# Kernel tuning notes

Measured on AMD Instinct MI355X. Metric: run time of the kernel, lower is better.

The kernel has to match this reference:

```python
import jax, jax.numpy as jnp
import numpy as np

NUM_HEADS = 4
KEY_DIM = 128


def rel_to_abs(rel):
    # rel: [B, heads, L, ww, 2*ww-1] -> [B, heads, L, ww, ww]
    B, heads, L, ww, dim = rel.shape
    flat = rel.reshape(B, heads, L, ww * (2 * ww - 1))[:, :, :, ww - 1:-1]
    return flat.reshape(B, heads, L, ww, 2 * (ww - 1))[..., :ww]


def relative_logits(pos_q, pos_emb_w, pos_emb_h):
    # pos_q: [B, hh, ww, heads, kd]
    # width logits
    q_w = jnp.transpose(pos_q, (0, 3, 1, 2, 4))           # [B, heads, hh, ww, kd]
    rel_w = jnp.einsum('bhxyd,dr->bhxyr', q_w, pos_emb_w)  # [B, heads, hh, ww, 2ww-1]
    rel_w = rel_to_abs(rel_w)                              # [B, heads, hh, ww, ww]
    # height logits
    q_h = jnp.transpose(pos_q, (0, 3, 2, 1, 4))           # [B, heads, ww, hh, kd]
    rel_h = jnp.einsum('bhyxd,dr->bhyxr', q_h, pos_emb_h)  # [B, heads, ww, hh, 2hh-1]
    rel_h = rel_to_abs(rel_h)                              # [B, heads, ww, hh, hh]
    rel_h = jnp.transpose(rel_h, (0, 1, 3, 2, 4))          # [B, heads, hh, ww, hh]
    # broadcast-add: [B, heads, hh, ww, hh, ww]
    return rel_w[:, :, :, :, None, :] + rel_h[:, :, :, :, :, None]


def setup_inputs() -> dict:
    key = jax.random.key(0)
    ks = jax.random.split(key, 7)
    B, H, W, C = 8, 32, 32, 512
    emb = NUM_HEADS * KEY_DIM
    stddev = KEY_DIM ** (-0.5)
    return {
        'x': jax.random.normal(ks[0], (B, H, W, C), jnp.float32),
        'Wq': jax.random.normal(ks[1], (C, emb), jnp.float32) * 0.02,
        'Wk': jax.random.normal(ks[2], (C, emb), jnp.float32) * 0.02,
        'Wv': jax.random.normal(ks[3], (C, emb), jnp.float32) * 0.02,
        'Wo': jax.random.normal(ks[4], (emb, emb), jnp.float32) * 0.02,
        'pos_emb_w': jax.random.normal(ks[5], (KEY_DIM, 2 * W - 1), jnp.float32) * stddev,
        'pos_emb_h': jax.random.normal(ks[6], (KEY_DIM, 2 * H - 1), jnp.float32) * stddev,
    }


def reference(x, Wq, Wk, Wv, Wo, pos_emb_w, pos_emb_h):
    B, hh, ww, C = x.shape
    heads, kd = NUM_HEADS, KEY_DIM
    L = hh * ww
    scale = 1.0 / jnp.sqrt(jnp.asarray(kd, x.dtype))

    q = (x @ Wq) * scale                                    # [B, hh, ww, heads*kd]
    attn_q = q.reshape(B, L, heads, kd).transpose(0, 2, 1, 3)   # [B, heads, L, kd]
    pos_q = q.reshape(B, hh, ww, heads, kd)
    k = (x @ Wk).reshape(B, L, heads, kd).transpose(0, 2, 3, 1)  # [B, heads, kd, L]
    v = (x @ Wv).reshape(B, L, heads, kd).transpose(0, 2, 1, 3)  # [B, heads, L, kd]

    scores = attn_q @ k                                      # [B, heads, L, L]
    pos = relative_logits(pos_q, pos_emb_w, pos_emb_h)        # [B, heads, hh, ww, hh, ww]
    scores = scores + pos.reshape(B, heads, L, L)
    attn = jax.nn.softmax(scores, axis=-1)

    out = attn @ v                                            # [B, heads, L, kd]
    out = out.transpose(0, 2, 1, 3).reshape(B, hh, ww, heads * kd)
    return out @ Wo
```

## Files before the change

kernel.cpp:

```cpp
#include <hip/hip_runtime.h>
#include <math.h>

typedef unsigned short u16;
typedef unsigned int u32;
typedef __bf16 bf16x8 __attribute__((ext_vector_type(8)));
typedef float f32x4 __attribute__((ext_vector_type(4)));

__device__ __forceinline__ u16 f2b(float f) {
  u32 u = __builtin_bit_cast(u32, f);
  u32 r = (u + 0x7FFFu + ((u >> 16) & 1u)) >> 16;
  return (u16)r;
}

__device__ __forceinline__ void glds16(const void* g, void* lds) {
  __builtin_amdgcn_global_load_lds(
      (const __attribute__((address_space(1))) void*)(void*)(const_cast<void*>(g)),
      (__attribute__((address_space(3))) void*)lds, 16, 0, 0);
}


__global__ __launch_bounds__(256) void castx(const float* __restrict__ x, u16* __restrict__ xb) {
  int idx = blockIdx.x * 256 + threadIdx.x;
  float4 v = ((const float4*)x)[idx];
  ushort4 o;
  o.x = f2b(v.x); o.y = f2b(v.y); o.z = f2b(v.z); o.w = f2b(v.w);
  ((ushort4*)xb)[idx] = o;
}

__global__ __launch_bounds__(256) void buildw(const float* __restrict__ Wq, const float* __restrict__ Wk,
                                              const float* __restrict__ Wv, const float* __restrict__ Wo,
                                              u16* __restrict__ WbigT, u16* __restrict__ WoT) {
  const float SCALE = 0.08838834764831845f;
  int row = blockIdx.x;
  int t = threadIdx.x;
  if (row < 512) {
    for (int k = t; k < 512; k += 256) WbigT[row*512 + k] = f2b(Wq[k*512 + row] * SCALE);
  } else if (row < 1024) {
    int n = row - 512;
    for (int k = t; k < 512; k += 256) WbigT[row*512 + k] = f2b(Wk[k*512 + n]);
  } else if (row < 1536) {
    int n = row - 1024;
    for (int k = t; k < 512; k += 256) WbigT[row*512 + k] = f2b(Wv[k*512 + n]);
  } else if (row < 1544) {
    int rr = row - 1536 + 2040;
    for (int k = t; k < 512; k += 256) WbigT[rr*512 + k] = 0;
  } else {
    int n = row - 1544;
    for (int k = t; k < 512; k += 256) WoT[n*512 + k] = f2b(Wo[k*512 + n]);
  }
}

__global__ __launch_bounds__(256) void wpe_kernel(const float* __restrict__ Wq, const float* __restrict__ pew,
                                                  const float* __restrict__ peh, u16* __restrict__ WbigT) {
  int k = blockIdx.x;
  int t = threadIdx.x;
  __shared__ float wrow[512];
  for (int j = t; j < 512; j += 256) wrow[j] = Wq[k*512 + j];
  __syncthreads();
  if (t < 252) {
    int h = t / 63, r = t - h*63;
    float aw = 0.f, ah = 0.f;
    for (int d = 0; d < 128; d++) {
      float qv = wrow[h*128 + d];
      aw += qv * pew[d*63 + r];
      ah += qv * peh[d*63 + r];
    }
    const float SCALE = 0.08838834764831845f;
    WbigT[(size_t)(1536 + t)*512 + k] = f2b(aw * SCALE);
    WbigT[(size_t)(1788 + t)*512 + k] = f2b(ah * SCALE);
  }
}

template<int MODE>
__global__ __launch_bounds__(256) void gemm_bt(
    const u16* __restrict__ A, const u16* __restrict__ Bt,
    float* __restrict__ outF,
    u16* __restrict__ Qb, u16* __restrict__ Kb, u16* __restrict__ Vt,
    float* __restrict__ RELW, float* __restrict__ RELH)
{
  __shared__ char sm[65536];
  const int tid = threadIdx.x;
  const int w = tid >> 6, l = tid & 63, g = l >> 4, c = l & 15;
  const int bm = blockIdx.x, bn = blockIdx.y;
  const int wm = (w >> 1) * 64, wn = (w & 1) * 64;

  f32x4 acc[4][4];
#pragma unroll
  for (int i = 0; i < 4; i++)
#pragma unroll
    for (int j = 0; j < 4; j++) acc[i][j] = f32x4{0.f, 0.f, 0.f, 0.f};

  const char* Ab = (const char*)A;
  const char* Bb = (const char*)Bt;
  const int rsub = l >> 3;
  const int csw = (((l & 7) ^ rsub) << 4);

#define G_STAGE(kb, p)                                                                    \
  {                                                                                       \
    char* As_ = sm + (p)*32768;                                                           \
    char* Bs_ = As_ + 16384;                                                              \
    const int kbyte = (kb) * 128;                                                         \
    _Pragma("unroll")                                                                     \
    for (int t = 0; t < 4; t++) {                                                         \
      const int row = (w*4 + t)*8 + rsub;                                                 \
      glds16(Ab + (size_t)(bm*128 + row) * 1024 + kbyte + csw, As_ + (w*4 + t)*1024);     \
      glds16(Bb + (size_t)(bn*128 + row) * 1024 + kbyte + csw, Bs_ + (w*4 + t)*1024);     \
    }                                                                                     \
  }

  G_STAGE(0, 0);
  G_STAGE(1, 1);

#pragma unroll
  for (int kb = 0; kb < 8; kb++) {
    const int p = kb & 1;
    if (kb < 7) { asm volatile("s_waitcnt vmcnt(8)" ::: "memory"); }
    else        { asm volatile("s_waitcnt vmcnt(0)" ::: "memory"); }
    __builtin_amdgcn_s_barrier();
    const char* As_ = sm + p*32768;
    const char* Bs_ = As_ + 16384;
#pragma unroll
    for (int ks = 0; ks < 2; ks++) {
      const int koff = (ks*64 + g*16) ^ ((c & 7) << 4);
      bf16x8 af[4], bfr[4];
#pragma unroll
      for (int mf = 0; mf < 4; mf++)
        af[mf] = *(const bf16x8*)(As_ + (wm + mf*16 + c)*128 + koff);
#pragma unroll
      for (int nf = 0; nf < 4; nf++)
        bfr[nf] = *(const bf16x8*)(Bs_ + (wn + nf*16 + c)*128 + koff);
#pragma unroll
      for (int mf = 0; mf < 4; mf++)
#pragma unroll
        for (int nf = 0; nf < 4; nf++)
          acc[mf][nf] = __builtin_amdgcn_mfma_f32_16x16x32_bf16(af[mf], bfr[nf], acc[mf][nf], 0, 0, 0);
    }
    __builtin_amdgcn_s_barrier();
    if (kb < 6) G_STAGE(kb + 2, p);
  }

  if (MODE == 0) {
#pragma unroll
    for (int mf = 0; mf < 4; mf++) {
#pragma unroll
      for (int nf = 0; nf < 4; nf++) {
        const int n = bn*128 + wn + nf*16 + c;
#pragma unroll
        for (int r = 0; r < 4; r++) {
          const int m = bm*128 + wm + mf*16 + g*4 + r;
          outF[(size_t)m*512 + n] = acc[mf][nf][r];
        }
      }
    }
  } else if (bn >= 8 && bn < 12) {
    char* T = sm;
#pragma unroll
    for (int mf = 0; mf < 4; mf++) {
#pragma unroll
      for (int nf = 0; nf < 4; nf++) {
        const int d2 = wn + nf*16 + c;
        const int swz = (d2 & 7) << 4;
#pragma unroll
        for (int r = 0; r < 4; r++) {
          const int i = wm + mf*16 + g*4 + r;
          *(u16*)(T + d2*256 + ((i*2) ^ swz)) = f2b(acc[mf][nf][r]);
        }
      }
    }
    __builtin_amdgcn_s_barrier();
    const int b = bm >> 3, h = bn - 8;
#pragma unroll
    for (int it = 0; it < 8; it++) {
      const int L = it*4096 + tid*16;
      const int d2 = L >> 8, kk = L & 255;
      const int swz = (d2 & 7) << 4;
      bf16x8 vv = *(const bf16x8*)(T + d2*256 + (kk ^ swz));
      char* dst = (char*)Vt + ((size_t)((b*4 + h)*128 + d2) * 1024 + (size_t)(bm & 7)*128) * 2 + kk;
      *(bf16x8*)dst = vv;
    }
  } else {
#pragma unroll
    for (int mf = 0; mf < 4; mf++) {
#pragma unroll
      for (int nf = 0; nf < 4; nf++) {
        const int n = bn*128 + wn + nf*16 + c;
#pragma unroll
        for (int r = 0; r < 4; r++) {
          const int m = bm*128 + wm + mf*16 + g*4 + r;
          const int b = m >> 10, i = m & 1023;
          const float v = acc[mf][nf][r];
          if (n < 512) {
            int h = n >> 7, d = n & 127;
            Qb[(size_t)((b*4 + h)*1024 + i)*128 + d] = f2b(v);
          } else if (n < 1024) {
            int h = (n - 512) >> 7, d = n & 127;
            Kb[(size_t)((b*4 + h)*1024 + i)*128 + d] = f2b(v);
          } else if (n >= 1536 && n < 1788) {
            int q = n - 1536, h = q / 63, r2 = q - h*63;
            RELW[(size_t)((b*4 + h)*1024 + i)*64 + r2] = v;
          } else if (n >= 1788 && n < 2040) {
            int q = n - 1788, h = q / 63, r2 = q - h*63;
            RELH[(size_t)((b*4 + h)*1024 + i)*64 + r2] = v;
          }
        }
      }
    }
  }
#undef G_STAGE
}

__global__ __launch_bounds__(256) void attn_fused(
    const u16* __restrict__ Qb, const u16* __restrict__ Kb, const u16* __restrict__ Vt,
    const float* __restrict__ RELW, const float* __restrict__ RELH,
    u16* __restrict__ AO)
{
  __shared__ char sm[73728];
  char* const Pl = sm + 65536;
  const int tid = threadIdx.x;
  const int w = tid >> 6, l = tid & 63, g = l >> 4, c = l & 15;
  const int bh = blockIdx.x, qt = blockIdx.y;
  const int i0 = qt * 64;

  bf16x8 qf[4];
  {
    const char* qbase = (const char*)Qb + (size_t)(bh*1024 + i0 + w*16 + c) * 256;
#pragma unroll
    for (int s = 0; s < 4; s++) qf[s] = *(const bf16x8*)(qbase + s*64 + g*16);
  }

  float xw0h[4], xw1h[4];
  const float* rhbase[4];
#pragma unroll
  for (int r = 0; r < 4; r++) {
    const int i = i0 + w*16 + g*4 + r;
    const int xi = i & 31, yi = i >> 5;
    const float* rw = RELW + ((size_t)(bh*1024 + i) << 6);
    xw0h[r] = rw[c - xi + 31];
    xw1h[r] = rw[c + 16 - xi + 31];
    rhbase[r] = RELH + ((size_t)(bh*1024 + i) << 6) + (31 - yi);
  }

  f32x4 Oacc[8];
#pragma unroll
  for (int fd = 0; fd < 8; fd++) Oacc[fd] = f32x4{0.f, 0.f, 0.f, 0.f};
  float mrow[4] = {-INFINITY, -INFINITY, -INFINITY, -INFINITY};
  float lrow[4] = {0.f, 0.f, 0.f, 0.f};

#define A_STAGE(jt, p)                                                                     \
  {                                                                                        \
    char* Kt_ = sm + (p)*32768;                                                            \
    char* Vs_ = Kt_ + 16384;                                                               \
    const int j0b = (jt) * 64;                                                             \
    _Pragma("unroll")                                                                      \
    for (int t = 0; t < 4; t++) {                                                          \
      const int L = (w*4 + t)*1024 + l*16;                                                 \
      const int jr = L >> 8, jb = L & 255;                                                 \
      glds16((const char*)Kb + (size_t)(bh*1024 + j0b + jr) * 256 + (jb ^ ((jr & 7) << 4)),\
             Kt_ + L);                                                                     \
      const int dr = L >> 7, db = L & 127;                                                 \
      glds16((const char*)Vt + (size_t)(bh*128 + dr) * 2048 + j0b*2 + (db ^ ((dr & 7) << 4)),\
             Vs_ + L);                                                                     \
    }                                                                                      \
  }

  A_STAGE(0, 0);
  A_STAGE(1, 1);

#pragma unroll 2
  for (int jt = 0; jt < 16; jt++) {
    const int p = jt & 1;
    if (jt < 15) { asm volatile("s_waitcnt vmcnt(8)" ::: "memory"); }
    else         { asm volatile("s_waitcnt vmcnt(0)" ::: "memory"); }
    __builtin_amdgcn_s_barrier();

    float yh0v[4], yh1v[4];
#pragma unroll
    for (int r = 0; r < 4; r++) { yh0v[r] = rhbase[r][jt*2]; yh1v[r] = rhbase[r][jt*2 + 1]; }

    const char* Kt_ = sm + p*32768;
    const char* Vs_ = Kt_ + 16384;

    f32x4 acc[4];
#pragma unroll
    for (int fn = 0; fn < 4; fn++) acc[fn] = f32x4{0.f, 0.f, 0.f, 0.f};
    __builtin_amdgcn_s_setprio(1);
#pragma unroll
    for (int s = 0; s < 4; s++) {
      const int koff = (s*64 + g*16) ^ ((c & 7) << 4);
#pragma unroll
      for (int fn = 0; fn < 4; fn++) {
        bf16x8 kf = *(const bf16x8*)(Kt_ + (fn*16 + c)*256 + koff);
        acc[fn] = __builtin_amdgcn_mfma_f32_16x16x32_bf16(qf[s], kf, acc[fn], 0, 0, 0);
      }
    }
    __builtin_amdgcn_s_setprio(0);

#pragma unroll
    for (int r = 0; r < 4; r++) {
      float mx = -INFINITY;
#pragma unroll
      for (int fn = 0; fn < 4; fn++) {
        float sb = acc[fn][r] + ((fn & 1) ? xw1h[r] : xw0h[r]) + ((fn >> 1) ? yh1v[r] : yh0v[r]);
        acc[fn][r] = sb;
        mx = fmaxf(mx, sb);
      }
      mx = fmaxf(mx, __shfl_xor(mx, 1));
      mx = fmaxf(mx, __shfl_xor(mx, 2));
      mx = fmaxf(mx, __shfl_xor(mx, 4));
      mx = fmaxf(mx, __shfl_xor(mx, 8));
      const float mnew = fmaxf(mrow[r], mx);
      const float sc = __expf(mrow[r] - mnew);
      mrow[r] = mnew;
      float ps = 0.f;
      const int rowl = g*4 + r;
      char* pb = Pl + w*2048 + rowl*128;
      const int swz = (rowl & 7) << 4;
#pragma unroll
      for (int fn = 0; fn < 4; fn++) {
        float pval = __expf(acc[fn][r] - mnew);
        ps += pval;
        *(u16*)(pb + (((fn*16 + c)*2) ^ swz)) = f2b(pval);
      }
      ps += __shfl_xor(ps, 1);
      ps += __shfl_xor(ps, 2);
      ps += __shfl_xor(ps, 4);
      ps += __shfl_xor(ps, 8);
      lrow[r] = lrow[r] * sc + ps;
#pragma unroll
      for (int fd = 0; fd < 8; fd++) Oacc[fd][r] *= sc;
    }

    __builtin_amdgcn_s_setprio(1);
#pragma unroll
    for (int s = 0; s < 2; s++) {
      const int koff = (s*64 + g*16) ^ ((c & 7) << 4);
      bf16x8 pf = *(const bf16x8*)(Pl + w*2048 + c*128 + koff);
#pragma unroll
      for (int fd = 0; fd < 8; fd++) {
        bf16x8 vf = *(const bf16x8*)(Vs_ + (fd*16 + c)*128 + koff);
        Oacc[fd] = __builtin_amdgcn_mfma_f32_16x16x32_bf16(pf, vf, Oacc[fd], 0, 0, 0);
      }
    }
    __builtin_amdgcn_s_setprio(0);

    __builtin_amdgcn_s_barrier();
    if (jt < 14) A_STAGE(jt + 2, p);
  }

  const int b = bh >> 2, h = bh & 3;
#pragma unroll
  for (int fd = 0; fd < 8; fd++) {
#pragma unroll
    for (int r = 0; r < 4; r++) {
      const int i = i0 + w*16 + g*4 + r;
      AO[(size_t)(b*1024 + i)*512 + h*128 + fd*16 + c] = f2b(Oacc[fd][r] / lrow[r]);
    }
  }
#undef A_STAGE
}

extern "C" void kernel_launch(void* const* d_in, const int* in_sizes, int n_in,
                              void* d_out, int out_size, void* d_ws, size_t ws_size,
                              hipStream_t stream) {
  const float* x   = (const float*)d_in[0];
  const float* Wq  = (const float*)d_in[1];
  const float* Wk  = (const float*)d_in[2];
  const float* Wv  = (const float*)d_in[3];
  const float* Wo  = (const float*)d_in[4];
  const float* pew = (const float*)d_in[5];
  const float* peh = (const float*)d_in[6];

  char* ws = (char*)d_ws;
  u16* xb    = (u16*)ws;    ws += (size_t)8192*512*2;
  u16* WbigT = (u16*)ws;    ws += (size_t)2048*512*2;
  u16* WoT   = (u16*)ws;    ws += (size_t)512*512*2;
  u16* Qb    = (u16*)ws;    ws += (size_t)32*1024*128*2;
  u16* Kb    = (u16*)ws;    ws += (size_t)32*1024*128*2;
  u16* Vt    = (u16*)ws;    ws += (size_t)32*1024*128*2;
  float* RELW = (float*)ws; ws += (size_t)32*1024*64*4;
  float* RELH = (float*)ws; ws += (size_t)32*1024*64*4;
  u16* AO    = (u16*)ws;    ws += (size_t)8192*512*2;

  castx<<<4096, 256, 0, stream>>>(x, xb);
  buildw<<<2056, 256, 0, stream>>>(Wq, Wk, Wv, Wo, WbigT, WoT);
  wpe_kernel<<<512, 256, 0, stream>>>(Wq, pew, peh, WbigT);
  gemm_bt<1><<<dim3(64, 16), 256, 0, stream>>>(xb, WbigT, nullptr, Qb, Kb, Vt, RELW, RELH);
  attn_fused<<<dim3(32, 16), 256, 0, stream>>>(Qb, Kb, Vt, RELW, RELH, AO);
  gemm_bt<0><<<dim3(64, 4), 256, 0, stream>>>(AO, WoT, (float*)d_out,
                                              nullptr, nullptr, nullptr, nullptr, nullptr);
}
```

Before: 114.9 us.

## Transpose QK^T MFMA so each lane owns one query row for softmax

Swaps the MFMA operand order so the score tile is transposed: each lane holds 16 scores of a single query row instead of 4 rows. The softmax max and sum then need only two cross-lane shuffles per tile instead of sixteen per row group, and a single running max and sum per lane. It also writes P with packed bf16 conversion and 8-byte LDS stores, and prefetches the height bias one tile ahead. In exchange, the per-row rescale factors and the final normalizer must be broadcast to the output layout through extra shuffles.

Measured after the change: 104.5 us. 9.0% less time.

```diff
diff --git a/kernel.cpp b/kernel.cpp
--- a/kernel.cpp
+++ b/kernel.cpp
@@ -228,23 +228,20 @@
     for (int s = 0; s < 4; s++) qf[s] = *(const bf16x8*)(qbase + s*64 + g*16);
   }
 
-  float xw0h[4], xw1h[4];
-  const float* rhbase[4];
-#pragma unroll
-  for (int r = 0; r < 4; r++) {
-    const int i = i0 + w*16 + g*4 + r;
-    const int xi = i & 31, yi = i >> 5;
-    const float* rw = RELW + ((size_t)(bh*1024 + i) << 6);
-    xw0h[r] = rw[c - xi + 31];
-    xw1h[r] = rw[c + 16 - xi + 31];
-    rhbase[r] = RELH + ((size_t)(bh*1024 + i) << 6) + (31 - yi);
-  }
+  const int i = i0 + w*16 + c;
+  const int xi = i & 31, yi = i >> 5;
+  const float* rw = RELW + ((size_t)(bh*1024 + i) << 6);
+  const float* rhb = RELH + ((size_t)(bh*1024 + i) << 6) + (31 - yi);
+  float xwh[2][4];
+#pragma unroll
+  for (int e = 0; e < 2; e++)
+#pragma unroll
+    for (int r = 0; r < 4; r++) xwh[e][r] = rw[e*16 + g*4 + r - xi + 31];
 
   f32x4 Oacc[8];
 #pragma unroll
   for (int fd = 0; fd < 8; fd++) Oacc[fd] = f32x4{0.f, 0.f, 0.f, 0.f};
-  float mrow[4] = {-INFINITY, -INFINITY, -INFINITY, -INFINITY};
-  float lrow[4] = {0.f, 0.f, 0.f, 0.f};
+  float m_q = -INFINITY, l_q = 0.f;
 
 #define A_STAGE(jt, p)                                                                     \
   {                                                                                        \
@@ -265,6 +262,7 @@
 
   A_STAGE(0, 0);
   A_STAGE(1, 1);
+  float yh0 = rhb[0], yh1 = rhb[1];
 
 #pragma unroll 2
   for (int jt = 0; jt < 16; jt++) {
@@ -273,10 +271,6 @@
     else         { asm volatile("s_waitcnt vmcnt(0)" ::: "memory"); }
     __builtin_amdgcn_s_barrier();
 
-    float yh0v[4], yh1v[4];
-#pragma unroll
-    for (int r = 0; r < 4; r++) { yh0v[r] = rhbase[r][jt*2]; yh1v[r] = rhbase[r][jt*2 + 1]; }
-
     const char* Kt_ = sm + p*32768;
     const char* Vs_ = Kt_ + 16384;
 
@@ -290,44 +284,62 @@
 #pragma unroll
       for (int fn = 0; fn < 4; fn++) {
         bf16x8 kf = *(const bf16x8*)(Kt_ + (fn*16 + c)*256 + koff);
-        acc[fn] = __builtin_amdgcn_mfma_f32_16x16x32_bf16(qf[s], kf, acc[fn], 0, 0, 0);
+        acc[fn] = __builtin_amdgcn_mfma_f32_16x16x32_bf16(kf, qf[s], acc[fn], 0, 0, 0);
       }
     }
     __builtin_amdgcn_s_setprio(0);
 
 #pragma unroll
+    for (int fn = 0; fn < 4; fn++)
+#pragma unroll
+      for (int r = 0; r < 4; r++)
+        acc[fn][r] += xwh[fn & 1][r] + ((fn >> 1) ? yh1 : yh0);
+
+    float mx = fmaxf(fmaxf(fmaxf(acc[0][0], acc[0][1]), fmaxf(acc[0][2], acc[0][3])),
+                     fmaxf(fmaxf(acc[1][0], acc[1][1]), fmaxf(acc[1][2], acc[1][3])));
+    mx = fmaxf(mx, fmaxf(fmaxf(fmaxf(acc[2][0], acc[2][1]), fmaxf(acc[2][2], acc[2][3])),
+                         fmaxf(fmaxf(acc[3][0], acc[3][1]), fmaxf(acc[3][2], acc[3][3]))));
+    mx = fmaxf(mx, __shfl_xor(mx, 16));
+    mx = fmaxf(mx, __shfl_xor(mx, 32));
+    const float mnew = fmaxf(m_q, mx);
+    const float scq = __expf(m_q - mnew);
+    m_q = mnew;
+
+    float pv[4][4];
+    float ps = 0.f;
+#pragma unroll
+    for (int fn = 0; fn < 4; fn++) {
+#pragma unroll
+      for (int r = 0; r < 4; r++) {
+        pv[fn][r] = __expf(acc[fn][r] - mnew);
+        ps += pv[fn][r];
+      }
+    }
+    ps += __shfl_xor(ps, 16);
+    ps += __shfl_xor(ps, 32);
+    l_q = l_q * scq + ps;
+
+    float nyh0 = 0.f, nyh1 = 0.f;
+    if (jt < 15) { nyh0 = rhb[(jt + 1)*2]; nyh1 = rhb[(jt + 1)*2 + 1]; }
+
+    {
+      char* pb = Pl + w*2048 + c*128;
+      const int swz = (c & 7) << 4;
+#pragma unroll
+      for (int fn = 0; fn < 4; fn++) {
+        u32 w0, w1;
+        asm("v_cvt_pk_bf16_f32 %0, %1, %2" : "=v"(w0) : "v"(pv[fn][0]), "v"(pv[fn][1]));
+        asm("v_cvt_pk_bf16_f32 %0, %1, %2" : "=v"(w1) : "v"(pv[fn][2]), "v"(pv[fn][3]));
+        uint2 pk; pk.x = w0; pk.y = w1;
+        *(uint2*)(pb + ((fn*32 + g*8) ^ swz)) = pk;
+      }
+    }
+
+#pragma unroll
     for (int r = 0; r < 4; r++) {
-      float mx = -INFINITY;
-#pragma unroll
-      for (int fn = 0; fn < 4; fn++) {
-        float sb = acc[fn][r] + ((fn & 1) ? xw1h[r] : xw0h[r]) + ((fn >> 1) ? yh1v[r] : yh0v[r]);
-        acc[fn][r] = sb;
-        mx = fmaxf(mx, sb);
-      }
-      mx = fmaxf(mx, __shfl_xor(mx, 1));
-      mx = fmaxf(mx, __shfl_xor(mx, 2));
-      mx = fmaxf(mx, __shfl_xor(mx, 4));
-      mx = fmaxf(mx, __shfl_xor(mx, 8));
-      const float mnew = fmaxf(mrow[r], mx);
-      const float sc = __expf(mrow[r] - mnew);
-      mrow[r] = mnew;
-      float ps = 0.f;
-      const int rowl = g*4 + r;
-      char* pb = Pl + w*2048 + rowl*128;
-      const int swz = (rowl & 7) << 4;
-#pragma unroll
-      for (int fn = 0; fn < 4; fn++) {
-        float pval = __expf(acc[fn][r] - mnew);
-        ps += pval;
-        *(u16*)(pb + (((fn*16 + c)*2) ^ swz)) = f2b(pval);
-      }
-      ps += __shfl_xor(ps, 1);
-      ps += __shfl_xor(ps, 2);
-      ps += __shfl_xor(ps, 4);
-      ps += __shfl_xor(ps, 8);
-      lrow[r] = lrow[r] * sc + ps;
-#pragma unroll
-      for (int fd = 0; fd < 8; fd++) Oacc[fd][r] *= sc;
+      const float scr = __shfl(scq, g*4 + r, 16);
+#pragma unroll
+      for (int fd = 0; fd < 8; fd++) Oacc[fd][r] *= scr;
     }
 
     __builtin_amdgcn_s_setprio(1);
@@ -345,15 +357,18 @@
 
     __builtin_amdgcn_s_barrier();
     if (jt < 14) A_STAGE(jt + 2, p);
+    yh0 = nyh0; yh1 = nyh1;
   }
 
   const int b = bh >> 2, h = bh & 3;
 #pragma unroll
-  for (int fd = 0; fd < 8; fd++) {
-#pragma unroll
-    for (int r = 0; r < 4; r++) {
-      const int i = i0 + w*16 + g*4 + r;
-      AO[(size_t)(b*1024 + i)*512 + h*128 + fd*16 + c] = f2b(Oacc[fd][r] / lrow[r]);
+  for (int r = 0; r < 4; r++) {
+    const float lr = __shfl(l_q, g*4 + r, 16);
+    const float linv = 1.0f / lr;
+    const int io = i0 + w*16 + g*4 + r;
+#pragma unroll
+    for (int fd = 0; fd < 8; fd++) {
+      AO[(size_t)(b*1024 + io)*512 + h*128 + fd*16 + c] = f2b(Oacc[fd][r] * linv);
     }
   }
 #undef A_STAGE
```
